# Performance work log

Hardware: AMD Instinct MI355X
Metric: run time of the kernel (lower is better)

Reference implementation:

```python
import jax, jax.numpy as jnp
import numpy as np

NUM_HEADS = 16
EPS = 1e-6


def setup_inputs() -> dict:
    key = jax.random.key(0)
    ks = jax.random.split(key, 7)
    B, N, C = 4, 2048, 1024
    s = 0.02
    return {
        "x": jax.random.normal(ks[0], (B, N, C), jnp.float32),
        "x_origin": jax.random.normal(ks[1], (B, N, C), jnp.float32),
        "decisions": jax.random.uniform(ks[2], (B, N), jnp.float32),
        "Wq": jax.random.normal(ks[3], (C, C), jnp.float32) * s,
        "Wk": jax.random.normal(ks[4], (C, C), jnp.float32) * s,
        "Wv": jax.random.normal(ks[5], (C, C), jnp.float32) * s,
        "Wp": jax.random.normal(ks[6], (C, C), jnp.float32) * s,
    }


def reference(x, x_origin, decisions, Wq, Wk, Wv, Wp):
    B, N, C = x.shape
    H = NUM_HEADS
    d = C // H
    scale = d ** (-0.5)

    # project and split heads: (B, H, N, d)
    q = (x @ Wq).reshape(B, N, H, d).transpose(0, 2, 1, 3)
    k = (x_origin @ Wk).reshape(B, N, H, d).transpose(0, 2, 1, 3)
    v = (x_origin @ Wv).reshape(B, N, H, d).transpose(0, 2, 1, 3)

    attn = jnp.einsum("bhnd,bhmd->bhnm", q, k) * scale  # (B, H, N, N)

    # policy-masked softmax with eps smoothing (softmax_with_policy)
    fuse_policy = (1.0 - decisions)[:, None, None, :]  # (B, 1, 1, N) over key axis
    max_att = jnp.max(attn, axis=-1, keepdims=True)
    e = jnp.exp(attn - max_att) * fuse_policy
    attn = (e + EPS / N) / (jnp.sum(e, axis=-1, keepdims=True) + EPS)

    out = jnp.einsum("bhnm,bhmd->bhnd", attn, v)  # (B, H, N, d)
    out = out.transpose(0, 2, 1, 3).reshape(B, N, C)
    return out @ Wp
```

## Files before the change

### kernel.cpp

```cpp
#include <hip/hip_runtime.h>

typedef unsigned short u16;
typedef __attribute__((ext_vector_type(8))) short bf16x8;
typedef __attribute__((ext_vector_type(4))) short s16x4;
typedef __attribute__((ext_vector_type(4))) float f32x4;

#define GLDS(g, l) __builtin_amdgcn_global_load_lds( \
    (const __attribute__((address_space(1))) unsigned int*)(g), \
    (__attribute__((address_space(3))) unsigned int*)(l), 16, 0, 0)

__device__ __forceinline__ u16 f2b(float f) {
  unsigned int x = __float_as_uint(f);
  return (u16)((x + 0x7fffu + ((x >> 16) & 1u)) >> 16);
}
__device__ __forceinline__ bf16x8 cvt8(float4 a, float4 b) {
  bf16x8 r;
  r[0] = (short)f2b(a.x); r[1] = (short)f2b(a.y);
  r[2] = (short)f2b(a.z); r[3] = (short)f2b(a.w);
  r[4] = (short)f2b(b.x); r[5] = (short)f2b(b.y);
  r[6] = (short)f2b(b.z); r[7] = (short)f2b(b.w);
  return r;
}

__global__ __launch_bounds__(256) void cvt_f32_bf16(const float* __restrict__ src,
                                                    u16* __restrict__ dst) {
  const int i0 = (blockIdx.x * 256 + threadIdx.x) * 8;
  const float4 a = *(const float4*)&src[i0];
  const float4 b = *(const float4*)&src[i0 + 4];
  *(bf16x8*)&dst[i0] = cvt8(a, b);
}

__global__ __launch_bounds__(256) void transpose_w4(
    const float* __restrict__ W0, const float* __restrict__ W1,
    const float* __restrict__ W2, const float* __restrict__ W3,
    u16* __restrict__ D0, u16* __restrict__ D1,
    u16* __restrict__ D2, u16* __restrict__ D3) {
  const int z = blockIdx.z;
  const float* W = (z == 0) ? W0 : (z == 1) ? W1 : (z == 2) ? W2 : W3;
  u16* Wt = (z == 0) ? D0 : (z == 1) ? D1 : (z == 2) ? D2 : D3;
  __shared__ u16 tile[32][33];
  const int tx = threadIdx.x & 31, ty = threadIdx.x >> 5;
  const int r0 = blockIdx.y * 32, c0 = blockIdx.x * 32;
#pragma unroll
  for (int i = 0; i < 32; i += 8)
    tile[ty + i][tx] = f2b(W[(r0 + ty + i) * 1024 + c0 + tx]);
  __syncthreads();
#pragma unroll
  for (int i = 0; i < 32; i += 8)
    Wt[(c0 + ty + i) * 1024 + r0 + tx] = tile[tx][ty + i];
}

template <int EPI, typename OT>
__global__ __launch_bounds__(256) void gemm_bt(const u16* __restrict__ A,
                                               const u16* __restrict__ Bt,
                                               OT* __restrict__ C,
                                               u16* __restrict__ C2) {
  __shared__ u16 As[2][128 * 32];
  __shared__ u16 Bs[2][128 * 32];
  const int t = threadIdx.x;
  const int wave = t >> 6, lane = t & 63;
  const int g = lane >> 4, a15 = lane & 15;
  const int wr = wave >> 1, wc = wave & 1;
  const int row0 = t >> 2;
  const int col0 = (t & 3) * 8;
  const int abase = (blockIdx.x * 128 + row0) * 1024 + col0;
  const int bbase = (blockIdx.y * 128 + row0) * 1024 + col0;

  f32x4 acc[4][4] = {};

  GLDS(A + abase, &As[0][wave * 512]);
  GLDS(A + abase + 64 * 1024, &As[0][2048 + wave * 512]);
  GLDS(Bt + bbase, &Bs[0][wave * 512]);
  GLDS(Bt + bbase + 64 * 1024, &Bs[0][2048 + wave * 512]);
  __syncthreads();

  for (int ki = 0; ki < 32; ++ki) {
    const int cur = ki & 1, nxt = cur ^ 1;
    const int ktn = (ki + 1) * 32;
    if (ki < 31) {
      GLDS(A + abase + ktn, &As[nxt][wave * 512]);
      GLDS(A + abase + 64 * 1024 + ktn, &As[nxt][2048 + wave * 512]);
      GLDS(Bt + bbase + ktn, &Bs[nxt][wave * 512]);
      GLDS(Bt + bbase + 64 * 1024 + ktn, &Bs[nxt][2048 + wave * 512]);
    }
    bf16x8 af[4], bfr[4];
#pragma unroll
    for (int mi = 0; mi < 4; ++mi)
      af[mi] = *(const bf16x8*)&As[cur][(wr * 64 + mi * 16 + a15) * 32 + g * 8];
#pragma unroll
    for (int ni = 0; ni < 4; ++ni)
      bfr[ni] = *(const bf16x8*)&Bs[cur][(wc * 64 + ni * 16 + a15) * 32 + g * 8];
#pragma unroll
    for (int mi = 0; mi < 4; ++mi)
#pragma unroll
      for (int ni = 0; ni < 4; ++ni)
        acc[mi][ni] = __builtin_amdgcn_mfma_f32_16x16x32_bf16(af[mi], bfr[ni], acc[mi][ni], 0, 0, 0);
    __syncthreads();
  }

  const int crow = blockIdx.x * 128 + wr * 64 + g * 4;
  const int ccol = blockIdx.y * 128 + wc * 64 + a15;
  if constexpr (EPI == 0) {
#pragma unroll
    for (int mi = 0; mi < 4; ++mi)
#pragma unroll
      for (int ni = 0; ni < 4; ++ni)
#pragma unroll
        for (int r = 0; r < 4; ++r) {
          const float v = acc[mi][ni][r];
          if constexpr (sizeof(OT) == 2)
            C[(crow + mi * 16 + r) * 1024 + ccol + ni * 16] = (OT)f2b(v);
          else
            C[(crow + mi * 16 + r) * 1024 + ccol + ni * 16] = (OT)v;
        }
  } else {
    if (blockIdx.y < 8) {
#pragma unroll
      for (int mi = 0; mi < 4; ++mi)
#pragma unroll
        for (int ni = 0; ni < 4; ++ni)
#pragma unroll
          for (int r = 0; r < 4; ++r)
            ((u16*)C)[(crow + mi * 16 + r) * 1024 + ccol + ni * 16] = f2b(acc[mi][ni][r]);
    } else {
#pragma unroll
      for (int mi = 0; mi < 4; ++mi) {
        const int n = crow + mi * 16;
        const int bq = n >> 11;
        const int nl = n & 2047;
#pragma unroll
        for (int ni = 0; ni < 4; ++ni) {
          const int c = ccol + ni * 16 - 1024;
          s16x4 v4;
          v4[0] = (short)f2b(acc[mi][ni][0]);
          v4[1] = (short)f2b(acc[mi][ni][1]);
          v4[2] = (short)f2b(acc[mi][ni][2]);
          v4[3] = (short)f2b(acc[mi][ni][3]);
          *(s16x4*)&C2[(((bq << 4) + (c >> 6)) * 64 + (c & 63)) * 2048 + nl] = v4;
        }
      }
    }
  }
}

__global__ __launch_bounds__(512) void attn_kernel(
    const u16* Q, const u16* __restrict__ K,
    const u16* __restrict__ Vt, const float* __restrict__ dec,
    u16* O) {
  const int f = blockIdx.x;
  const int bh = (f & 7) * 8 + ((f >> 3) & 7);
  const int qx = f >> 6;
  const int b = bh >> 4, h = bh & 15;
  __shared__ u16 K_lds[2][64 * 64];
  __shared__ u16 V_lds[2][64 * 64];
  __shared__ __align__(16) u16 P_lds[8][32 * 72];
  __shared__ float l2p_lds[2048];

  const int wave = threadIdx.x >> 6, lane = threadIdx.x & 63;
  const int g = lane >> 4, a15 = lane & 15;
  u16* pl = &P_lds[wave][0];

  {
    const int i0 = threadIdx.x * 4;
    const float4 d0 = *(const float4*)&dec[b * 2048 + i0];
    float4 o0;
    o0.x = __log2f(fmaxf(1.f - d0.x, 1e-38f));
    o0.y = __log2f(fmaxf(1.f - d0.y, 1e-38f));
    o0.z = __log2f(fmaxf(1.f - d0.z, 1e-38f));
    o0.w = __log2f(fmaxf(1.f - d0.w, 1e-38f));
    *(float4*)&l2p_lds[i0] = o0;
  }

  bf16x8 qf[2][2];
  {
    const int qr = (b * 2048 + qx * 256 + wave * 32 + a15) * 1024 + h * 64 + g * 8;
#pragma unroll
    for (int qg = 0; qg < 2; ++qg) {
      qf[qg][0] = *(const bf16x8*)&Q[qr + qg * 16 * 1024];
      qf[qg][1] = *(const bf16x8*)&Q[qr + qg * 16 * 1024 + 32];
    }
  }

  const int srow = lane >> 3;
  const int swze = (((lane & 7) * 16) ^ (srow << 4)) >> 1;
  const u16* Kg = K + ((size_t)(b * 2048 + wave * 8 + srow)) * 1024 + h * 64 + swze;
  const u16* Vg = Vt + ((size_t)(bh * 64 + wave * 8 + srow)) * 2048 + swze;
  u16* kdst[2] = {&K_lds[0][wave * 8 * 64], &K_lds[1][wave * 8 * 64]};
  u16* vdst[2] = {&V_lds[0][wave * 8 * 64], &V_lds[1][wave * 8 * 64]};

  GLDS(Kg, kdst[0]);
  GLDS(Vg, vdst[0]);
  __syncthreads();

  const float CSC = 0.125f * 1.44269504f;
  f32x4 acc[2][4] = {};
  f32x4 ls[2] = {};

  for (int it = 0; it < 32; ++it) {
    const int cur = it & 1, nxt = cur ^ 1;
    if (it < 31) {
      const int ktn = (it + 1) * 64;
      GLDS(Kg + (size_t)ktn * 1024, kdst[nxt]);
      GLDS(Vg + ktn, vdst[nxt]);
    }
    const int kt = it * 64;
    f32x4 sf[2][4];
#pragma unroll
    for (int sub = 0; sub < 4; ++sub) {
      const int krow = sub * 16 + a15;
      const char* kp = (const char*)&K_lds[cur][krow * 64];
      const int swz = (krow & 7) << 4;
      const bf16x8 k0 = *(const bf16x8*)(kp + ((g * 16) ^ swz));
      const bf16x8 k1 = *(const bf16x8*)(kp + ((g * 16 + 64) ^ swz));
#pragma unroll
      for (int qg = 0; qg < 2; ++qg) {
        f32x4 s = {0.f, 0.f, 0.f, 0.f};
        s = __builtin_amdgcn_mfma_f32_16x16x32_bf16(k0, qf[qg][0], s, 0, 0, 0);
        s = __builtin_amdgcn_mfma_f32_16x16x32_bf16(k1, qf[qg][1], s, 0, 0, 0);
        sf[qg][sub] = s;
      }
    }
#pragma unroll
    for (int qg = 0; qg < 2; ++qg) {
#pragma unroll
      for (int sub = 0; sub < 4; ++sub) {
        const float4 lp = *(const float4*)&l2p_lds[kt + sub * 16 + g * 4];
        const float e0 = __builtin_amdgcn_exp2f(fmaf(sf[qg][sub][0], CSC, lp.x));
        const float e1 = __builtin_amdgcn_exp2f(fmaf(sf[qg][sub][1], CSC, lp.y));
        const float e2 = __builtin_amdgcn_exp2f(fmaf(sf[qg][sub][2], CSC, lp.z));
        const float e3 = __builtin_amdgcn_exp2f(fmaf(sf[qg][sub][3], CSC, lp.w));
        ls[qg][0] += e0; ls[qg][1] += e1; ls[qg][2] += e2; ls[qg][3] += e3;
        unsigned int w0, w1;
        asm("v_cvt_pk_bf16_f32 %0, %1, %2" : "=v"(w0) : "v"(e0), "v"(e1));
        asm("v_cvt_pk_bf16_f32 %0, %1, %2" : "=v"(w1) : "v"(e2), "v"(e3));
        uint2 w; w.x = w0; w.y = w1;
        *(uint2*)&pl[(qg * 16 + a15) * 72 + sub * 16 + g * 4] = w;
      }
    }
    asm volatile("" ::: "memory");
#pragma unroll
    for (int kc = 0; kc < 2; ++kc) {
      const bf16x8 pa0 = *(const bf16x8*)&pl[a15 * 72 + kc * 32 + g * 8];
      const bf16x8 pa1 = *(const bf16x8*)&pl[(16 + a15) * 72 + kc * 32 + g * 8];
#pragma unroll
      for (int ni = 0; ni < 4; ++ni) {
        const int vrow = ni * 16 + a15;
        const char* vp = (const char*)&V_lds[cur][vrow * 64];
        const int vswz = (vrow & 7) << 4;
        const bf16x8 vb = *(const bf16x8*)(vp + ((kc * 64 + g * 16) ^ vswz));
        acc[0][ni] = __builtin_amdgcn_mfma_f32_16x16x32_bf16(pa0, vb, acc[0][ni], 0, 0, 0);
        acc[1][ni] = __builtin_amdgcn_mfma_f32_16x16x32_bf16(pa1, vb, acc[1][ni], 0, 0, 0);
      }
    }
    __syncthreads();
  }
#pragma unroll
  for (int qg = 0; qg < 2; ++qg) {
    float lsum = (ls[qg][0] + ls[qg][1]) + (ls[qg][2] + ls[qg][3]);
    lsum += __shfl_xor(lsum, 16);
    lsum += __shfl_xor(lsum, 32);
    const float li0 = 1.f / (__shfl(lsum, g * 4 + 0) + 1e-30f);
    const float li1 = 1.f / (__shfl(lsum, g * 4 + 1) + 1e-30f);
    const float li2 = 1.f / (__shfl(lsum, g * 4 + 2) + 1e-30f);
    const float li3 = 1.f / (__shfl(lsum, g * 4 + 3) + 1e-30f);
    const int obase = (b * 2048 + qx * 256 + wave * 32 + qg * 16 + g * 4) * 1024 + h * 64 + a15;
#pragma unroll
    for (int ni = 0; ni < 4; ++ni) {
      O[obase + 0 * 1024 + ni * 16] = f2b(acc[qg][ni][0] * li0);
      O[obase + 1 * 1024 + ni * 16] = f2b(acc[qg][ni][1] * li1);
      O[obase + 2 * 1024 + ni * 16] = f2b(acc[qg][ni][2] * li2);
      O[obase + 3 * 1024 + ni * 16] = f2b(acc[qg][ni][3] * li3);
    }
  }
}

extern "C" void kernel_launch(void* const* d_in, const int* in_sizes, int n_in,
                              void* d_out, int out_size, void* d_ws, size_t ws_size,
                              hipStream_t stream) {
  (void)in_sizes; (void)n_in; (void)out_size; (void)ws_size;
  const float* x   = (const float*)d_in[0];
  const float* xo  = (const float*)d_in[1];
  const float* dec = (const float*)d_in[2];
  const float* Wq  = (const float*)d_in[3];
  const float* Wk  = (const float*)d_in[4];
  const float* Wv  = (const float*)d_in[5];
  const float* Wp  = (const float*)d_in[6];
  float* out = (float*)d_out;

  char* ws = (char*)d_ws;
  u16* Wqt  = (u16*)(ws + ((size_t)0 << 20));
  u16* Wkvt = (u16*)(ws + ((size_t)2 << 20));
  u16* Wpt  = (u16*)(ws + ((size_t)6 << 20));
  u16* Qb   = (u16*)(ws + ((size_t)8 << 20));
  u16* Vtb  = (u16*)(ws + ((size_t)24 << 20));
  u16* Kb   = (u16*)d_out;
  u16* Xb   = (u16*)((char*)d_out + ((size_t)16 << 20));

  const dim3 blk(256);
  transpose_w4<<<dim3(32, 32, 4), blk, 0, stream>>>(
      Wq, Wk, Wv, Wp, Wqt, Wkvt, Wkvt + 1024 * 1024, Wpt);

  cvt_f32_bf16<<<dim3(4096), blk, 0, stream>>>(xo, Xb);
  gemm_bt<2, u16><<<dim3(64, 16), blk, 0, stream>>>(Xb, Wkvt, Kb, Vtb);

  cvt_f32_bf16<<<dim3(4096), blk, 0, stream>>>(x, Xb);
  gemm_bt<0, u16><<<dim3(64, 8), blk, 0, stream>>>(Xb, Wqt, Qb, nullptr);

  attn_kernel<<<dim3(512), dim3(512), 0, stream>>>(Qb, Kb, Vtb, dec, Qb);

  gemm_bt<0, float><<<dim3(64, 8), blk, 0, stream>>>(Qb, Wpt, out, nullptr);
}
```

Measured before the change: 223.2 us.

## Fuse Q and KV projections into one GEMM launch with inline x conversion

The Q projection and the KV projection now run in a single launch over a 64x24 grid, with blocks choosing their weight matrix and output by blockIdx.y. For the Q part, the fp32 x tile is loaded straight from global memory into registers and converted to bf16 while the MFMA work proceeds, which removes the separate x conversion kernel and its bf16 round trip. This saves one conversion launch and one GEMM launch and lets more blocks run concurrently. In exchange, the Q blocks read fp32 data through ordinary loads, which costs more bandwidth and registers than the asynchronous global-to-LDS loads the KV blocks use.

New measurement: 199.3 us. -10.7%, faster.

```diff
diff --git a/kernel.cpp b/kernel.cpp
--- a/kernel.cpp
+++ b/kernel.cpp
@@ -50,11 +50,122 @@
     Wt[(c0 + ty + i) * 1024 + r0 + tx] = tile[tx][ty + i];
 }
 
-template <int EPI, typename OT>
-__global__ __launch_bounds__(256) void gemm_bt(const u16* __restrict__ A,
-                                               const u16* __restrict__ Bt,
-                                               OT* __restrict__ C,
-                                               u16* __restrict__ C2) {
+__global__ __launch_bounds__(256) void gemm_fused(
+    const float* __restrict__ Ax, const u16* __restrict__ Axo,
+    const u16* __restrict__ Wqt, const u16* __restrict__ Wkvt,
+    u16* __restrict__ Qb, u16* __restrict__ Kb, u16* __restrict__ Vtb) {
+  __shared__ u16 As[2][128 * 32];
+  __shared__ u16 Bs[2][128 * 32];
+  const int t = threadIdx.x;
+  const int wave = t >> 6, lane = t & 63;
+  const int g = lane >> 4, a15 = lane & 15;
+  const int wr = wave >> 1, wc = wave & 1;
+  const int row0 = t >> 2;
+  const int col0 = (t & 3) * 8;
+  const int y = blockIdx.y;
+  const bool qpart = (y < 8);
+  const u16* Bt = qpart ? Wqt : Wkvt;
+  const int yb = qpart ? y : (y - 8);
+  const int abase = (blockIdx.x * 128 + row0) * 1024 + col0;
+  const int bbase = (yb * 128 + row0) * 1024 + col0;
+
+  f32x4 acc[4][4] = {};
+
+  GLDS(Bt + bbase, &Bs[0][wave * 512]);
+  GLDS(Bt + bbase + 64 * 1024, &Bs[0][2048 + wave * 512]);
+  if (qpart) {
+    const float* Ag = Ax + abase;
+    const float4 x0 = *(const float4*)(Ag);
+    const float4 x1 = *(const float4*)(Ag + 4);
+    const float4 y0 = *(const float4*)(Ag + 64 * 1024);
+    const float4 y1 = *(const float4*)(Ag + 64 * 1024 + 4);
+    *(bf16x8*)&As[0][row0 * 32 + col0] = cvt8(x0, x1);
+    *(bf16x8*)&As[0][(row0 + 64) * 32 + col0] = cvt8(y0, y1);
+  } else {
+    GLDS(Axo + abase, &As[0][wave * 512]);
+    GLDS(Axo + abase + 64 * 1024, &As[0][2048 + wave * 512]);
+  }
+  __syncthreads();
+
+  for (int ki = 0; ki < 32; ++ki) {
+    const int cur = ki & 1, nxt = cur ^ 1;
+    const int ktn = (ki + 1) * 32;
+    const bool pf = ki < 31;
+    float4 x0, x1, y0, y1;
+    if (pf) {
+      GLDS(Bt + bbase + ktn, &Bs[nxt][wave * 512]);
+      GLDS(Bt + bbase + 64 * 1024 + ktn, &Bs[nxt][2048 + wave * 512]);
+      if (qpart) {
+        const float* Ag = Ax + abase + ktn;
+        x0 = *(const float4*)(Ag);
+        x1 = *(const float4*)(Ag + 4);
+        y0 = *(const float4*)(Ag + 64 * 1024);
+        y1 = *(const float4*)(Ag + 64 * 1024 + 4);
+      } else {
+        GLDS(Axo + abase + ktn, &As[nxt][wave * 512]);
+        GLDS(Axo + abase + 64 * 1024 + ktn, &As[nxt][2048 + wave * 512]);
+      }
+    }
+    bf16x8 af[4], bfr[4];
+#pragma unroll
+    for (int mi = 0; mi < 4; ++mi)
+      af[mi] = *(const bf16x8*)&As[cur][(wr * 64 + mi * 16 + a15) * 32 + g * 8];
+#pragma unroll
+    for (int ni = 0; ni < 4; ++ni)
+      bfr[ni] = *(const bf16x8*)&Bs[cur][(wc * 64 + ni * 16 + a15) * 32 + g * 8];
+#pragma unroll
+    for (int mi = 0; mi < 4; ++mi)
+#pragma unroll
+      for (int ni = 0; ni < 4; ++ni)
+        acc[mi][ni] = __builtin_amdgcn_mfma_f32_16x16x32_bf16(af[mi], bfr[ni], acc[mi][ni], 0, 0, 0);
+    if (pf && qpart) {
+      *(bf16x8*)&As[nxt][row0 * 32 + col0] = cvt8(x0, x1);
+      *(bf16x8*)&As[nxt][(row0 + 64) * 32 + col0] = cvt8(y0, y1);
+    }
+    __syncthreads();
+  }
+
+  const int crow = blockIdx.x * 128 + wr * 64 + g * 4;
+  const int ccol = yb * 128 + wc * 64 + a15;
+  if (qpart) {
+#pragma unroll
+    for (int mi = 0; mi < 4; ++mi)
+#pragma unroll
+      for (int ni = 0; ni < 4; ++ni)
+#pragma unroll
+        for (int r = 0; r < 4; ++r)
+          Qb[(crow + mi * 16 + r) * 1024 + ccol + ni * 16] = f2b(acc[mi][ni][r]);
+  } else if (yb < 8) {
+#pragma unroll
+    for (int mi = 0; mi < 4; ++mi)
+#pragma unroll
+      for (int ni = 0; ni < 4; ++ni)
+#pragma unroll
+        for (int r = 0; r < 4; ++r)
+          Kb[(crow + mi * 16 + r) * 1024 + ccol + ni * 16] = f2b(acc[mi][ni][r]);
+  } else {
+#pragma unroll
+    for (int mi = 0; mi < 4; ++mi) {
+      const int n = crow + mi * 16;
+      const int bq = n >> 11;
+      const int nl = n & 2047;
+#pragma unroll
+      for (int ni = 0; ni < 4; ++ni) {
+        const int c = ccol + ni * 16 - 1024;
+        s16x4 v4;
+        v4[0] = (short)f2b(acc[mi][ni][0]);
+        v4[1] = (short)f2b(acc[mi][ni][1]);
+        v4[2] = (short)f2b(acc[mi][ni][2]);
+        v4[3] = (short)f2b(acc[mi][ni][3]);
+        *(s16x4*)&Vtb[(((bq << 4) + (c >> 6)) * 64 + (c & 63)) * 2048 + nl] = v4;
+      }
+    }
+  }
+}
+
+__global__ __launch_bounds__(256) void gemm_out(const u16* __restrict__ A,
+                                                const u16* __restrict__ Bt,
+                                                float* __restrict__ C) {
   __shared__ u16 As[2][128 * 32];
   __shared__ u16 Bs[2][128 * 32];
   const int t = threadIdx.x;
@@ -100,47 +211,13 @@
 
   const int crow = blockIdx.x * 128 + wr * 64 + g * 4;
   const int ccol = blockIdx.y * 128 + wc * 64 + a15;
-  if constexpr (EPI == 0) {
-#pragma unroll
-    for (int mi = 0; mi < 4; ++mi)
-#pragma unroll
-      for (int ni = 0; ni < 4; ++ni)
-#pragma unroll
-        for (int r = 0; r < 4; ++r) {
-          const float v = acc[mi][ni][r];
-          if constexpr (sizeof(OT) == 2)
-            C[(crow + mi * 16 + r) * 1024 + ccol + ni * 16] = (OT)f2b(v);
-          else
-            C[(crow + mi * 16 + r) * 1024 + ccol + ni * 16] = (OT)v;
-        }
-  } else {
-    if (blockIdx.y < 8) {
-#pragma unroll
-      for (int mi = 0; mi < 4; ++mi)
-#pragma unroll
-        for (int ni = 0; ni < 4; ++ni)
-#pragma unroll
-          for (int r = 0; r < 4; ++r)
-            ((u16*)C)[(crow + mi * 16 + r) * 1024 + ccol + ni * 16] = f2b(acc[mi][ni][r]);
-    } else {
-#pragma unroll
-      for (int mi = 0; mi < 4; ++mi) {
-        const int n = crow + mi * 16;
-        const int bq = n >> 11;
-        const int nl = n & 2047;
-#pragma unroll
-        for (int ni = 0; ni < 4; ++ni) {
-          const int c = ccol + ni * 16 - 1024;
-          s16x4 v4;
-          v4[0] = (short)f2b(acc[mi][ni][0]);
-          v4[1] = (short)f2b(acc[mi][ni][1]);
-          v4[2] = (short)f2b(acc[mi][ni][2]);
-          v4[3] = (short)f2b(acc[mi][ni][3]);
-          *(s16x4*)&C2[(((bq << 4) + (c >> 6)) * 64 + (c & 63)) * 2048 + nl] = v4;
-        }
-      }
-    }
-  }
+#pragma unroll
+  for (int mi = 0; mi < 4; ++mi)
+#pragma unroll
+    for (int ni = 0; ni < 4; ++ni)
+#pragma unroll
+      for (int r = 0; r < 4; ++r)
+        C[(crow + mi * 16 + r) * 1024 + ccol + ni * 16] = acc[mi][ni][r];
 }
 
 __global__ __launch_bounds__(512) void attn_kernel(
@@ -301,12 +378,10 @@
       Wq, Wk, Wv, Wp, Wqt, Wkvt, Wkvt + 1024 * 1024, Wpt);
 
   cvt_f32_bf16<<<dim3(4096), blk, 0, stream>>>(xo, Xb);
-  gemm_bt<2, u16><<<dim3(64, 16), blk, 0, stream>>>(Xb, Wkvt, Kb, Vtb);
-
-  cvt_f32_bf16<<<dim3(4096), blk, 0, stream>>>(x, Xb);
-  gemm_bt<0, u16><<<dim3(64, 8), blk, 0, stream>>>(Xb, Wqt, Qb, nullptr);
+
+  gemm_fused<<<dim3(64, 24), blk, 0, stream>>>(x, Xb, Wqt, Wkvt, Qb, Kb, Vtb);
 
   attn_kernel<<<dim3(512), dim3(512), 0, stream>>>(Qb, Kb, Vtb, dec, Qb);
 
-  gemm_bt<0, float><<<dim3(64, 8), blk, 0, stream>>>(Qb, Wpt, out, nullptr);
-}
+  gemm_out<<<dim3(64, 8), blk, 0, stream>>>(Qb, Wpt, out);
+}
```
